# Optimization experiments

Hardware: AMD Instinct MI355X
Metric: run time of the kernel (lower is better)

## Reference

```python
import jax, jax.numpy as jnp
import numpy as np

H = 16      # query heads
KV = 8      # kv heads
D = 128     # head_dim
HID = 2048  # hidden_size
T = 2048    # tokens
EPS = 1e-6
THETA = 1000000.0


def setup_inputs() -> dict:
    key = jax.random.key(0)
    ks = jax.random.split(key, 4)
    return {
        "hidden_states": jax.random.normal(ks[0], (T, HID), jnp.float32),
        "positions": jnp.arange(T, dtype=jnp.int32),
        "qkv_w": jax.random.normal(ks[1], (H * D + 2 * KV * D, HID), jnp.float32) * 0.02,
        "o_w": jax.random.normal(ks[2], (HID, H * D), jnp.float32) * 0.02,
        "q_norm_w": jnp.ones((D,), jnp.float32),
        "k_norm_w": jnp.ones((D,), jnp.float32),
    }


def _rmsnorm(x, w):
    # x: [T, heads, D]; normalize over last dim
    var = jnp.mean(x * x, axis=-1, keepdims=True)
    return x * jax.lax.rsqrt(var + EPS) * w


def _rope(x, positions):
    # neox-style rotate-half; x: [T, heads, D]
    half = D // 2
    inv_freq = 1.0 / (THETA ** (jnp.arange(0, half, dtype=jnp.float32) / half * 1.0))
    inv_freq = 1.0 / (THETA ** (jnp.arange(0, D, 2, dtype=jnp.float32) / D))
    ang = positions.astype(jnp.float32)[:, None] * inv_freq  # [T, D/2]
    cos = jnp.cos(ang)[:, None, :]
    sin = jnp.sin(ang)[:, None, :]
    x1, x2 = x[..., :half], x[..., half:]
    return jnp.concatenate([x1 * cos - x2 * sin, x2 * cos + x1 * sin], axis=-1)


def reference(hidden_states, positions, qkv_w, o_w, q_norm_w, k_norm_w):
    scale = D ** -0.5
    qkv = hidden_states @ qkv_w.T  # [T, H*D + 2*KV*D]
    q = qkv[:, : H * D].reshape(T, H, D)
    k = qkv[:, H * D : H * D + KV * D].reshape(T, KV, D)
    v = qkv[:, H * D + KV * D :].reshape(T, KV, D)

    q = _rope(_rmsnorm(q, q_norm_w), positions)
    k = _rope(_rmsnorm(k, k_norm_w), positions)

    # GQA: repeat kv heads to match query heads
    rep = H // KV
    k = jnp.repeat(k, rep, axis=1)  # [T, H, D]
    v = jnp.repeat(v, rep, axis=1)

    scores = jnp.einsum("thd,shd->hts", q, k) * scale  # [H, T, T]
    causal = positions[:, None] >= positions[None, :]  # [T, T]
    scores = jnp.where(causal[None, :, :], scores, jnp.float32(-1e30))
    p = jax.nn.softmax(scores, axis=-1)
    o = jnp.einsum("hts,shd->thd", p, v).reshape(T, H * D)
    return o @ o_w.T  # [T, HID]
```

## Files before the change

kernel.cpp:

```cpp
#include <hip/hip_runtime.h>
#include <math.h>

#define T_TOK 2048
#define HID 2048
#define NH 16
#define NKV 8
#define HD 128
#define QKV_N 4096
#define EPS 1e-6f

typedef unsigned short u16;
typedef unsigned int   u32;
typedef __attribute__((ext_vector_type(8))) u16   u16x8;
typedef __attribute__((ext_vector_type(8))) short short8;
typedef __attribute__((ext_vector_type(4))) float floatx4;
typedef __attribute__((ext_vector_type(16))) float f32x16;
typedef __attribute__((ext_vector_type(4))) u32   u32x4;

__device__ __forceinline__ u16 f2bf(float x) {
    u32 u = __float_as_uint(x);
    u = (u + 0x7fffu + ((u >> 16) & 1u)) >> 16;
    return (u16)u;
}
__device__ __forceinline__ float bf2f(u16 h) {
    return __uint_as_float(((u32)h) << 16);
}
__device__ __forceinline__ u32 cvtpk_bf16(float lo, float hi) {
    u32 r;
    asm("v_cvt_pk_bf16_f32 %0, %1, %2" : "=v"(r) : "v"(lo), "v"(hi));
    return r;
}

__device__ __forceinline__ void cvt8(const float* __restrict__ in,
                                     u16* __restrict__ out, size_t i)
{
    float4 a = *(const float4*)(in + i);
    float4 b = *(const float4*)(in + i + 4);
    u16x8 o;
    o[0] = f2bf(a.x); o[1] = f2bf(a.y); o[2] = f2bf(a.z); o[3] = f2bf(a.w);
    o[4] = f2bf(b.x); o[5] = f2bf(b.y); o[6] = f2bf(b.z); o[7] = f2bf(b.w);
    *(u16x8*)(out + i) = o;
}

__global__ __launch_bounds__(256) void cvt_pair(
    const float* __restrict__ ina, u16* __restrict__ outa,
    const float* __restrict__ inb, u16* __restrict__ outb)
{
    const int bid = blockIdx.x;
    if (bid < 2048) cvt8(ina, outa, ((size_t)bid * 256 + threadIdx.x) * 8);
    else            cvt8(inb, outb, ((size_t)(bid - 2048) * 256 + threadIdx.x) * 8);
}

#define GBM 256
#define GBN 128
#define GBK 64
#define BUFSH 24576

#define WAITV6 asm volatile("s_waitcnt vmcnt(6)" ::: "memory")
#define WAITV0 asm volatile("s_waitcnt vmcnt(0)" ::: "memory")
#define LGKM0  asm volatile("s_waitcnt lgkmcnt(0)" ::: "memory")
#define BARR   asm volatile("s_barrier" ::: "memory")
#define SB     __builtin_amdgcn_sched_barrier(0)

#define STAGEU(i, tt, dstb) \
    __builtin_amdgcn_global_load_lds( \
        (const __attribute__((address_space(1))) u32*)(gsrc[i] + (size_t)(tt)*GBK), \
        (__attribute__((address_space(3))) u32*)((dstb) + loff[i]), 16, 0, 0)

#define RD_A(dst, srcb, f) do { \
    dst[0] = *(const short8*)((srcb) + arow + (f)*1024 + achunk0); \
    dst[1] = *(const short8*)((srcb) + arow + (f)*1024 + achunk1); } while (0)

#define RD_B(dst, srcb) do { \
    _Pragma("unroll") \
    for (int j_ = 0; j_ < 4; ++j_) { \
        dst[j_][0] = *(const short8*)((srcb) + 16384 + brow + j_*1024 + achunk0); \
        dst[j_][1] = *(const short8*)((srcb) + 16384 + brow + j_*1024 + achunk1); } } while (0)

#define MM(f, aa, bb) do { \
    __builtin_amdgcn_s_setprio(1); \
    _Pragma("unroll") \
    for (int j_ = 0; j_ < 4; ++j_) { \
        acc[f][j_] = __builtin_amdgcn_mfma_f32_16x16x32_bf16(aa[0], bb[j_][0], acc[f][j_], 0, 0, 0); \
        acc[f][j_] = __builtin_amdgcn_mfma_f32_16x16x32_bf16(aa[1], bb[j_][1], acc[f][j_], 0, 0, 0); } \
    __builtin_amdgcn_s_setprio(0); } while (0)

#define TILE(t, CURB, NXTB, THDB, BBC, BBN) do { \
    const bool st_ = (t) + 2 < nt; \
    if (st_) { STAGEU(0, (t)+2, THDB); STAGEU(1, (t)+2, THDB); } \
    RD_A(aP1, CURB, 1); SB; \
    MM(0, aP0, BBC); SB; \
    if (st_) { STAGEU(2, (t)+2, THDB); STAGEU(3, (t)+2, THDB); } \
    RD_A(aP0, CURB, 2); SB; \
    MM(1, aP1, BBC); SB; \
    if (st_) { STAGEU(4, (t)+2, THDB); STAGEU(5, (t)+2, THDB); } \
    RD_A(aP1, CURB, 3); SB; \
    MM(2, aP0, BBC); \
    if ((t) + 1 < nt) { \
        if (st_) { WAITV6; } else { WAITV0; } \
        LGKM0; BARR; SB; \
        RD_B(BBN, NXTB); RD_A(aP0, NXTB, 0); \
    } \
    SB; \
    MM(3, aP1, BBC); SB; \
} while (0)

template<bool OUT_BF16>
__global__ __launch_bounds__(512, 2) void gemm_bt_8p(
    const u16* __restrict__ A, const u16* __restrict__ B,
    void* __restrict__ Cv, int K, int lda, int ldb, int ldc)
{
    extern __shared__ short lds[];
    const int tid = threadIdx.x;
    const int w  = tid >> 6;
    const int l  = tid & 63;
    const int m0 = blockIdx.y * GBM;
    const int n0 = blockIdx.x * GBN;
    const int mr = (w >> 1) * 64;
    const int nc = (w & 1) * 64;
    const int cc = l & 15;
    const int q4 = l >> 4;

    const int lr = l >> 3;
    const int gchunk = ((l & 7) ^ (lr & 7)) * 8;
    const u16* gsrc[6]; int loff[6];
    #pragma unroll
    for (int i = 0; i < 6; ++i) {
        const int u = w * 6 + i;
        if (u < 32) {
            gsrc[i] = A + (size_t)(m0 + u*8 + lr) * lda + gchunk;
            loff[i] = u * 512;
        } else {
            const int v = u - 32;
            gsrc[i] = B + (size_t)(n0 + v*8 + lr) * ldb + gchunk;
            loff[i] = 16384 + v * 512;
        }
    }

    const int achunk0 = ((q4)     ^ (cc & 7)) * 8;
    const int achunk1 = ((4 + q4) ^ (cc & 7)) * 8;
    const int arow = (mr + cc) * 64;
    const int brow = (nc + cc) * 64;

    floatx4 acc[4][4];
    #pragma unroll
    for (int f = 0; f < 4; ++f)
        #pragma unroll
        for (int j = 0; j < 4; ++j) acc[f][j] = (floatx4){0.f, 0.f, 0.f, 0.f};

    short8 aP0[2], aP1[2], bbE[4][2], bbO[4][2];
    short* b0 = lds;
    short* b1 = lds + BUFSH;
    short* b2 = lds + 2 * BUFSH;
    const int nt = K >> 6;

    #pragma unroll
    for (int i = 0; i < 6; ++i) STAGEU(i, 0, b0);
    #pragma unroll
    for (int i = 0; i < 6; ++i) STAGEU(i, 1, b1);
    WAITV6; BARR; SB;
    RD_B(bbE, b0); RD_A(aP0, b0, 0);

    short *CURB = b0, *NXTB = b1, *THDB = b2;
    for (int t = 0; t < nt; t += 2) {
        TILE(t, CURB, NXTB, THDB, bbE, bbO);
        { short* tmp = CURB; CURB = NXTB; NXTB = THDB; THDB = tmp; }
        TILE(t + 1, CURB, NXTB, THDB, bbO, bbE);
        { short* tmp = CURB; CURB = NXTB; NXTB = THDB; THDB = tmp; }
    }

    const int r0 = q4 * 4;
    #pragma unroll
    for (int f = 0; f < 4; ++f)
        #pragma unroll
        for (int j = 0; j < 4; ++j)
            #pragma unroll
            for (int r = 0; r < 4; ++r) {
                const int row = m0 + mr + f*16 + r0 + r;
                const int col = n0 + nc + j*16 + cc;
                if (OUT_BF16)
                    ((u16*)Cv)[(size_t)row * ldc + col] = f2bf(acc[f][j][r]);
                else
                    ((float*)Cv)[(size_t)row * ldc + col] = acc[f][j][r];
            }
}

__global__ __launch_bounds__(256) void prep(
    u16* __restrict__ qkv, const int* __restrict__ positions,
    const float* __restrict__ qw, const float* __restrict__ kw,
    u16* __restrict__ Kp, u16* __restrict__ Vtp)
{
    const int bid = blockIdx.x;
    const int tile = bid & 31, kvh = bid >> 5;
    const int tid = threadIdx.x;
    const int w = tid >> 6, l = tid & 63;
    const int t0 = tile * 64;

    const float qw0 = qw[2*l], qw1 = qw[2*l+1];
    const float kw0 = kw[2*l], kw1 = kw[2*l+1];
    const int   i0  = (2*l) & 63;
    const float if0 = exp2f(-(float)i0     * 0.311430758895690f);
    const float if1 = exp2f(-(float)(i0+1) * 0.311430758895690f);

    for (int rr = w; rr < 64; rr += 4) {
        const int t = t0 + rr;
        const int pos = positions[t];
        const float a0 = (float)pos * if0;
        const float a1 = (float)pos * if1;
        const float s0 = sinf(a0), c0 = cosf(a0);
        const float s1 = sinf(a1), c1 = cosf(a1);

        #pragma unroll
        for (int pass = 0; pass < 3; ++pass) {
            const int off = (pass < 2) ? (2*kvh + pass)*HD : NH*HD + kvh*HD;
            const float w0 = (pass < 2) ? qw0 : kw0;
            const float w1 = (pass < 2) ? qw1 : kw1;
            u16* p = qkv + (size_t)t*QKV_N + off;

            const u32 pk = *(const u32*)(p + 2*l);
            const float x0 = bf2f((u16)pk), x1 = bf2f((u16)(pk >> 16));
            float ss = x0*x0 + x1*x1;
            #pragma unroll
            for (int x = 1; x < 64; x <<= 1) ss += __shfl_xor(ss, x);
            const float rs = rsqrtf(ss * (1.0f/128.0f) + EPS);
            const float xn0 = x0 * rs * w0, xn1 = x1 * rs * w1;
            const float px0 = __shfl_xor(xn0, 32);
            const float px1 = __shfl_xor(xn1, 32);

            float o0, o1;
            if (l < 32) { o0 = xn0*c0 - px0*s0; o1 = xn1*c1 - px1*s1; }
            else        { o0 = xn0*c0 + px0*s0; o1 = xn1*c1 + px1*s1; }
            const u32 outpk = (u32)f2bf(o0) | ((u32)f2bf(o1) << 16);

            if (pass < 2) {
                *(u32*)(p + 2*l) = outpk;
            } else {
                const int ch = l >> 2;
                u16* dst = Kp + ((size_t)(kvh*32 + tile)*64 + rr)*128
                              + (ch ^ (rr & 15))*8 + (l & 3)*2;
                *(u32*)dst = outpk;
            }
        }
    }

    __shared__ u16 tl[64][136];
    {
        const int t  = tid >> 2;
        const int c0 = (tid & 3) * 32;
        const u16* src = qkv + (size_t)(t0 + t)*QKV_N + NH*HD + NKV*HD + kvh*HD + c0;
        #pragma unroll
        for (int p2 = 0; p2 < 4; ++p2)
            *(u16x8*)(&tl[t][c0 + p2*8]) = *(const u16x8*)(src + p2*8);
    }
    __syncthreads();
    {
        u16* dstb = Vtp + (size_t)(kvh*64 + tile*2) * 4096;
        #pragma unroll
        for (int i = 0; i < 4; ++i) {
            const int id = tid*4 + i;
            const int d = id >> 3;
            const int o = id & 7;
            u16x8 v;
            #pragma unroll
            for (int j = 0; j < 8; ++j) v[j] = tl[o*8 + j][d];
            *(u16x8*)(dstb + (o >> 2)*4096 + d*32 + (((o & 3) ^ (d & 3)))*8) = v;
        }
    }
}

__global__ __launch_bounds__(256, 4) void attn_mfma32(
    const u16* __restrict__ qkv, const u16* __restrict__ Kp,
    const u16* __restrict__ Vtp,
    u16* __restrict__ P0, u16* __restrict__ P1,
    u16* __restrict__ P2, u16* __restrict__ P3,
    float2* __restrict__ ml)
{
    const int id   = blockIdx.x;
    const int kvh  = id & 7;
    const int u    = id >> 3;
    const int hp   = u & 1;
    const int part = (u >> 1) & 3;
    const int q4b  = u >> 3;
    const int g    = q4b & 3;
    const int s4   = q4b >> 2;
    const int qt   = (s4 & 1) ? (2*g + (s4 >> 1)) : ((15 - (s4 >> 1)) - 2*g);
    const int h    = kvh*2 + hp;
    const int t0q  = qt * 128;

    const int tid = threadIdx.x;
    const int w   = tid >> 6;
    const int l   = tid & 63;
    const int q31 = l & 31;
    const int hi  = l >> 5;

    __shared__ short Ks[2][4096];
    __shared__ short Vts[2][4096];

    short8 qf[8];
    {
        const u16* qrow = qkv + (size_t)(t0q + w*32 + q31) * QKV_N + h*HD;
        #pragma unroll
        for (int ks = 0; ks < 8; ++ks)
            qf[ks] = *(const short8*)(qrow + ks*16 + hi*8);
    }

    float m_run = -3.0e38f, l_run = 0.f;
    f32x16 accO[4];
    #pragma unroll
    for (int nd = 0; nd < 4; ++nd)
        #pragma unroll
        for (int r = 0; r < 16; ++r) accO[nd][r] = 0.f;

    const float Cs = 0.12751744f;

    const int tlo = part * (qt + 1);
    const int thi = tlo + (qt + 1);

    auto issue = [&](int t32, int buf) {
        const size_t tb = (size_t)(kvh*64 + t32) * 4096;
        const u16* g2 = ((w < 2) ? Kp : Vtp) + tb + (w & 1)*2048 + l*8;
        short* p = ((w < 2) ? Ks[buf] : Vts[buf]) + (w & 1)*2048 + l*8;
        #pragma unroll
        for (int i = 0; i < 4; ++i)
            __builtin_amdgcn_global_load_lds(
                (const __attribute__((address_space(1))) u32*)(g2 + i*512),
                (__attribute__((address_space(3))) u32*)(p + i*512), 16, 0, 0);
    };

    issue(tlo, 0);
    int cur = 0;

    for (int tt = tlo; tt < thi; ++tt) {
        __syncthreads();
        if (tt + 1 < thi) issue(tt + 1, cur ^ 1);

        const short* Kc = Ks[cur];
        const short* Vc = Vts[cur];

        f32x16 accS;
        #pragma unroll
        for (int r = 0; r < 16; ++r) accS[r] = 0.f;

        __builtin_amdgcn_s_setprio(1);
        #pragma unroll
        for (int ks = 0; ks < 8; ++ks) {
            short8 a = *(const short8*)(Kc + q31*128 + ((2*ks + hi) ^ (q31 & 15))*8);
            accS = __builtin_amdgcn_mfma_f32_32x32x16_bf16(a, qf[ks], accS, 0, 0, 0);
        }
        __builtin_amdgcn_s_setprio(0);

        if (tt >= 4*qt) {
            const int kvb0 = tt*32 + (hi << 2);
            const int qg_g = t0q + w*32 + q31;
            #pragma unroll
            for (int r = 0; r < 16; ++r) {
                const int kvg = kvb0 + (r&3) + 8*(r>>2);
                if (kvg > qg_g) accS[r] = -1.0e30f;
            }
        }

        float mx = accS[0];
        #pragma unroll
        for (int r = 1; r < 16; ++r) mx = fmaxf(mx, accS[r]);
        mx = fmaxf(mx, __shfl_xor(mx, 32));

        if (__any(mx > m_run + 11.76f)) {
            const float m_new = fmaxf(m_run, mx);
            const float alpha = exp2f((m_run - m_new) * Cs);
            l_run *= alpha;
            m_run = m_new;
            #pragma unroll
            for (int r = 0; r < 16; ++r) {
                const float ar = __shfl(alpha, ((r&3) + 8*(r>>2)) + (hi<<2));
                accO[0][r] *= ar; accO[1][r] *= ar;
                accO[2][r] *= ar; accO[3][r] *= ar;
            }
        }
        const float mb = m_run * Cs;
        float lsum = 0.f;
        #pragma unroll
        for (int r = 0; r < 16; ++r) {
            const float e = exp2f(accS[r]*Cs - mb);
            accS[r] = e;
            lsum += e;
        }
        lsum += __shfl_xor(lsum, 32);
        l_run += lsum;

        short8 aP[2];
        #pragma unroll
        for (int ks2 = 0; ks2 < 2; ++ks2) {
            const int R = ks2 * 8;
            u32 x0 = cvtpk_bf16(accS[R+0], accS[R+1]);
            u32 x1 = cvtpk_bf16(accS[R+2], accS[R+3]);
            u32 x2 = cvtpk_bf16(accS[R+4], accS[R+5]);
            u32 x3 = cvtpk_bf16(accS[R+6], accS[R+7]);
            asm("v_permlane32_swap_b32 %0, %1" : "+v"(x0), "+v"(x2));
            asm("v_permlane32_swap_b32 %0, %1" : "+v"(x1), "+v"(x3));
            u32x4 aw; aw.x = x0; aw.y = x1; aw.z = x2; aw.w = x3;
            aP[ks2] = __builtin_bit_cast(short8, aw);
        }

        __builtin_amdgcn_s_setprio(1);
        #pragma unroll
        for (int ks2 = 0; ks2 < 2; ++ks2) {
            #pragma unroll
            for (int nd = 0; nd < 4; ++nd) {
                short8 bv = *(const short8*)(Vc + (nd*32 + q31)*32
                                             + ((ks2*2 + hi) ^ (q31 & 3))*8);
                accO[nd] = __builtin_amdgcn_mfma_f32_32x32x16_bf16(aP[ks2], bv, accO[nd], 0, 0, 0);
            }
        }
        __builtin_amdgcn_s_setprio(0);

        cur ^= 1;
    }

    u16* Op = (part == 0) ? P0 : (part == 1) ? P1 : (part == 2) ? P2 : P3;
    const size_t hb = (size_t)h * T_TOK;
    #pragma unroll
    for (int r = 0; r < 16; ++r) {
        const int qr = (r&3) + 8*(r>>2) + (hi<<2);
        u16* op = Op + (hb + t0q + w*32 + qr) * HD;
        op[q31]      = f2bf(accO[0][r]);
        op[32 + q31] = f2bf(accO[1][r]);
        op[64 + q31] = f2bf(accO[2][r]);
        op[96 + q31] = f2bf(accO[3][r]);
    }
    if (l < 32)
        ml[(size_t)part*NH*T_TOK + hb + t0q + w*32 + l]
            = make_float2(m_run, l_run);
}

__global__ __launch_bounds__(256) void combine4_cvt(
    const u16* __restrict__ P0, const u16* __restrict__ P1,
    const u16* __restrict__ P2, const u16* __restrict__ P3,
    const float2* __restrict__ ml, u16* __restrict__ qkv,
    const float* __restrict__ ow, u16* __restrict__ owbf)
{
    const int bid = blockIdx.x;
    if (bid >= 2048) {
        cvt8(ow, owbf, ((size_t)(bid - 2048) * 256 + threadIdx.x) * 8);
        return;
    }
    const int idx = bid * 256 + threadIdx.x;
    const int c16 = idx & 15;
    const int t   = (idx >> 4) & (T_TOK - 1);
    const int h   = idx >> 15;
    const size_t base = (size_t)h * T_TOK + t;
    const size_t NT = (size_t)NH * T_TOK;
    const float2 a = ml[base];
    const float2 b = ml[base + NT];
    const float2 c = ml[base + 2*NT];
    const float2 d = ml[base + 3*NT];
    const float Cs = 0.12751744f;
    const float mM = fmaxf(fmaxf(a.x, b.x), fmaxf(c.x, d.x));
    const float wA = exp2f((a.x - mM) * Cs);
    const float wB = exp2f((b.x - mM) * Cs);
    const float wC = exp2f((c.x - mM) * Cs);
    const float wD = exp2f((d.x - mM) * Cs);
    const float inv = 1.0f / (wA*a.y + wB*b.y + wC*c.y + wD*d.y);
    const u16x8 A = *(const u16x8*)(P0 + base * HD + c16*8);
    const u16x8 B = *(const u16x8*)(P1 + base * HD + c16*8);
    const u16x8 C = *(const u16x8*)(P2 + base * HD + c16*8);
    const u16x8 D = *(const u16x8*)(P3 + base * HD + c16*8);
    u16x8 o;
    #pragma unroll
    for (int j = 0; j < 8; ++j)
        o[j] = f2bf((wA*bf2f(A[j]) + wB*bf2f(B[j]) + wC*bf2f(C[j]) + wD*bf2f(D[j])) * inv);
    *(u16x8*)(qkv + (size_t)t * QKV_N + h * HD + c16*8) = o;
}

extern "C" void kernel_launch(void* const* d_in, const int* in_sizes, int n_in,
                              void* d_out, int out_size, void* d_ws, size_t ws_size,
                              hipStream_t stream)
{
    const float* hidden    = (const float*)d_in[0];
    const int*   positions = (const int*)  d_in[1];
    const float* qkv_w     = (const float*)d_in[2];
    const float* o_w       = (const float*)d_in[3];
    const float* q_norm_w  = (const float*)d_in[4];
    const float* k_norm_w  = (const float*)d_in[5];
    float* out = (float*)d_out;

    u16* qkvbf = (u16*)d_ws;
    u16* wbf   = qkvbf + (size_t)T_TOK * QKV_N;
    u16* abf   = wbf   + (size_t)QKV_N * HID;
    u16* kpb   = abf   + (size_t)T_TOK * HID;
    u16* vpb   = kpb   + (size_t)NKV * T_TOK * HD;

    u16* P0 = wbf;
    u16* P1 = wbf + (size_t)NH * T_TOK * HD;
    u16* P2 = abf;
    u16* P3 = (u16*)out;
    float2* mlp = (float2*)((u16*)out + (size_t)NH * T_TOK * HD);

    static bool s_attr = false;
    if (!s_attr) {
        (void)hipFuncSetAttribute(
            reinterpret_cast<const void*>(&gemm_bt_8p<true>),
            hipFuncAttributeMaxDynamicSharedMemorySize, 147456);
        (void)hipFuncSetAttribute(
            reinterpret_cast<const void*>(&gemm_bt_8p<false>),
            hipFuncAttributeMaxDynamicSharedMemorySize, 147456);
        s_attr = true;
    }

    cvt_pair<<<6144, 256, 0, stream>>>(hidden, abf, qkv_w, wbf);

    gemm_bt_8p<true><<<dim3(QKV_N/GBN, T_TOK/GBM), 512, 147456, stream>>>(
        abf, wbf, qkvbf, HID, HID, HID, QKV_N);

    prep<<<256, 256, 0, stream>>>(qkvbf, positions, q_norm_w, k_norm_w, kpb, vpb);

    attn_mfma32<<<1024, 256, 0, stream>>>(qkvbf, kpb, vpb, P0, P1, P2, P3, mlp);

    combine4_cvt<<<4096, 256, 0, stream>>>(P0, P1, P2, P3, mlp, qkvbf, o_w, kpb);

    gemm_bt_8p<false><<<dim3(HID/GBN, T_TOK/GBM), 512, 147456, stream>>>(
        qkvbf, kpb, out, HID, QKV_N, HID, HID);
}
```

Measured before the change: 272.0 us.

## Split-K the output projection GEMM in two and add partials

The output projection GEMM launches a second slice along grid z, so each slice covers half of K and writes its fp32 partial to a separate buffer (reusing the weight workspace). A new elementwise kernel then adds the two partials. The grid of 16x8=128 blocks was too small to fill the GPU, and doubling the block count is meant to improve occupancy. The cost is an extra kernel launch and one extra read/write pass over the 16 MB output. Separately, the attention kernel's launch-bounds occupancy hint drops from 4 to 3, which gives each thread more registers.

Measured after the change: 251.9 us. 1.08x faster.

```diff
diff --git a/kernel.cpp b/kernel.cpp
--- a/kernel.cpp
+++ b/kernel.cpp
@@ -49,6 +49,20 @@
     const int bid = blockIdx.x;
     if (bid < 2048) cvt8(ina, outa, ((size_t)bid * 256 + threadIdx.x) * 8);
     else            cvt8(inb, outb, ((size_t)(bid - 2048) * 256 + threadIdx.x) * 8);
+}
+
+__global__ __launch_bounds__(256) void addf32(
+    float* __restrict__ out, const float* __restrict__ part)
+{
+    const size_t i = ((size_t)blockIdx.x * 256 + threadIdx.x) * 8;
+    float4 a0 = *(const float4*)(out + i);
+    float4 a1 = *(const float4*)(out + i + 4);
+    float4 b0 = *(const float4*)(part + i);
+    float4 b1 = *(const float4*)(part + i + 4);
+    a0.x += b0.x; a0.y += b0.y; a0.z += b0.z; a0.w += b0.w;
+    a1.x += b1.x; a1.y += b1.y; a1.z += b1.z; a1.w += b1.w;
+    *(float4*)(out + i)     = a0;
+    *(float4*)(out + i + 4) = a1;
 }
 
 #define GBM 256
@@ -108,7 +122,8 @@
 template<bool OUT_BF16>
 __global__ __launch_bounds__(512, 2) void gemm_bt_8p(
     const u16* __restrict__ A, const u16* __restrict__ B,
-    void* __restrict__ Cv, int K, int lda, int ldb, int ldc)
+    void* __restrict__ Cv, void* __restrict__ Cv2,
+    int Ks, int lda, int ldb, int ldc)
 {
     extern __shared__ short lds[];
     const int tid = threadIdx.x;
@@ -116,6 +131,10 @@
     const int l  = tid & 63;
     const int m0 = blockIdx.y * GBM;
     const int n0 = blockIdx.x * GBN;
+    const int z  = blockIdx.z;
+    A += (size_t)z * Ks;
+    B += (size_t)z * Ks;
+    void* Cw = z ? Cv2 : Cv;
     const int mr = (w >> 1) * 64;
     const int nc = (w & 1) * 64;
     const int cc = l & 15;
@@ -152,7 +171,7 @@
     short* b0 = lds;
     short* b1 = lds + BUFSH;
     short* b2 = lds + 2 * BUFSH;
-    const int nt = K >> 6;
+    const int nt = Ks >> 6;
 
     #pragma unroll
     for (int i = 0; i < 6; ++i) STAGEU(i, 0, b0);
@@ -179,9 +198,9 @@
                 const int row = m0 + mr + f*16 + r0 + r;
                 const int col = n0 + nc + j*16 + cc;
                 if (OUT_BF16)
-                    ((u16*)Cv)[(size_t)row * ldc + col] = f2bf(acc[f][j][r]);
+                    ((u16*)Cw)[(size_t)row * ldc + col] = f2bf(acc[f][j][r]);
                 else
-                    ((float*)Cv)[(size_t)row * ldc + col] = acc[f][j][r];
+                    ((float*)Cw)[(size_t)row * ldc + col] = acc[f][j][r];
             }
 }
 
@@ -268,7 +287,7 @@
     }
 }
 
-__global__ __launch_bounds__(256, 4) void attn_mfma32(
+__global__ __launch_bounds__(256, 3) void attn_mfma32(
     const u16* __restrict__ qkv, const u16* __restrict__ Kp,
     const u16* __restrict__ Vtp,
     u16* __restrict__ P0, u16* __restrict__ P1,
@@ -494,6 +513,7 @@
     u16* P2 = abf;
     u16* P3 = (u16*)out;
     float2* mlp = (float2*)((u16*)out + (size_t)NH * T_TOK * HD);
+    float* partC = (float*)wbf;
 
     static bool s_attr = false;
     if (!s_attr) {
@@ -508,8 +528,8 @@
 
     cvt_pair<<<6144, 256, 0, stream>>>(hidden, abf, qkv_w, wbf);
 
-    gemm_bt_8p<true><<<dim3(QKV_N/GBN, T_TOK/GBM), 512, 147456, stream>>>(
-        abf, wbf, qkvbf, HID, HID, HID, QKV_N);
+    gemm_bt_8p<true><<<dim3(QKV_N/GBN, T_TOK/GBM, 1), 512, 147456, stream>>>(
+        abf, wbf, qkvbf, qkvbf, HID, HID, HID, QKV_N);
 
     prep<<<256, 256, 0, stream>>>(qkvbf, positions, q_norm_w, k_norm_w, kpb, vpb);
 
@@ -517,6 +537,8 @@
 
     combine4_cvt<<<4096, 256, 0, stream>>>(P0, P1, P2, P3, mlp, qkvbf, o_w, kpb);
 
-    gemm_bt_8p<false><<<dim3(HID/GBN, T_TOK/GBM), 512, 147456, stream>>>(
-        qkvbf, kpb, out, HID, QKV_N, HID, HID);
-}
+    gemm_bt_8p<false><<<dim3(HID/GBN, T_TOK/GBM, 2), 512, 147456, stream>>>(
+        qkvbf, kpb, out, partC, HID/2, QKV_N, HID, HID);
+
+    addf32<<<(T_TOK*HID)/2048, 256, 0, stream>>>(out, partC);
+}
```
